# Optimization experiments

Hardware: AMD Instinct MI355X
Metric: run time of the kernel (lower is better)

## Reference

```python
import jax, jax.numpy as jnp
import numpy as np

NODE_NUM = 1_000_000
TYPE_NUM = 4
DIM = 128
L = 80
K = 5
M = 5
B = 256
LK = L - K  # 75


def setup_inputs() -> dict:
    key = jax.random.key(0)
    ks = jax.random.split(key, 8)
    walk = jax.random.randint(ks[0], (B, LK), 0, NODE_NUM)
    pos = jax.random.randint(ks[1], (B, LK, K), 0, NODE_NUM)
    neg = jax.random.randint(ks[2], (B, LK, K, M), 0, NODE_NUM)
    walk_type = jax.random.randint(ks[3], (B, LK), 0, TYPE_NUM)
    pos_type = jax.random.randint(ks[4], (B, LK, K), 0, TYPE_NUM)
    neg_type = jax.random.randint(ks[5], (B, LK, K, M), 0, TYPE_NUM)
    node_embedding = 0.1 * jax.random.normal(ks[6], (NODE_NUM, DIM), dtype=jnp.float32)
    relationship_embedding = jax.random.normal(ks[7], (TYPE_NUM * TYPE_NUM, DIM), dtype=jnp.float32)
    return {
        'walk': walk, 'pos': pos, 'neg': neg,
        'walk_type': walk_type, 'pos_type': pos_type, 'neg_type': neg_type,
        'node_embedding': node_embedding,
        'relationship_embedding': relationship_embedding,
    }


def reference(walk, pos, neg, walk_type, pos_type, neg_type, node_embedding, relationship_embedding):
    T = TYPE_NUM
    # pair type indices into relationship table
    pos_pair_type = T * walk_type[:, :, None] + pos_type               # [B,LK,K]
    neg_pair_type = T * walk_type[:, :, None, None] + neg_type          # [B,LK,K,M]
    pos_pair = relationship_embedding[pos_pair_type]                    # [B,LK,K,D]
    neg_pair = relationship_embedding[neg_pair_type]                    # [B,LK,K,M,D]
    # per-offset pair-type ids (offset by window position k)
    ar = jnp.arange(K)
    pos_pair_type_out = T * T * ar[None, None, :] + pos_pair_type       # [B,LK,K]
    neg_pair_type_out = T * T * ar[None, None, :, None] + neg_pair_type  # [B,LK,K,M]
    # flatten K*M negative dim
    neg_flat = neg.reshape(B, LK, K * M)
    neg_pair = neg_pair.reshape(B, LK, K * M, DIM)
    # embedding gathers
    walk_e = node_embedding[walk]        # [B,LK,D]
    pos_e = node_embedding[pos]          # [B,LK,K,D]
    neg_e = node_embedding[neg_flat]     # [B,LK,K*M,D]
    # sigmoid gate + dot product against walk embedding
    pos_g = pos_e * jax.nn.sigmoid(pos_pair)
    neg_g = neg_e * jax.nn.sigmoid(neg_pair)
    pos_score = jnp.einsum('bld,blkd->blk', walk_e, pos_g).reshape(-1)
    neg_score = jnp.einsum('bld,blkd->blk', walk_e, neg_g).reshape(-1)
    return (pos_score, neg_score, pos_pair_type_out.reshape(-1), neg_pair_type_out.reshape(-1))
```

## Files before the change

### kernel.cpp

```cpp
#include <hip/hip_runtime.h>
#include <math.h>

constexpr int NODE_NUM = 1000000;
constexpr int TYPE_NUM = 4;
constexpr int DIM      = 128;
constexpr int K        = 5;
constexpr int M        = 5;
constexpr int B        = 256;
constexpr int LK       = 75;
constexpr int NBL      = B * LK;
constexpr int PS       = NBL * K;
constexpr int NS       = NBL * K * M;


__global__ __launch_bounds__(256) void skipgram_kernel(
    const int*   __restrict__ walk,
    const int*   __restrict__ pos,
    const int*   __restrict__ neg,
    const int*   __restrict__ walk_type,
    const int*   __restrict__ pos_type,
    const int*   __restrict__ neg_type,
    const float* __restrict__ node_emb,
    const float* __restrict__ rel_emb,
    float*       __restrict__ out)
{
    __shared__ float sig[TYPE_NUM * TYPE_NUM * DIM];
    const int tid = threadIdx.x;
    for (int i = tid; i < TYPE_NUM * TYPE_NUM * DIM; i += 256) {
        const float x = rel_emb[i];
        sig[i] = 1.0f / (1.0f + expf(-x));
    }
    __syncthreads();

    const int wave = tid >> 6;
    const int lane = tid & 63;
    const int half = lane >> 5;
    const int hl   = lane & 31;

    int idx = blockIdx.x * 4 + wave;
    idx = __builtin_amdgcn_readfirstlane(idx);

    const int wnode = walk[idx];
    const int wt    = walk_type[idx];

    const float4 we = *(const float4*)(node_emb + (size_t)wnode * DIM + 4 * hl);


    int tpA[15], tpB[15];
    #pragma unroll
    for (int j = 0; j < 15; ++j) {
        const int r0 = 2 * j, r1 = 2 * j + 1;
        tpA[j] = (r0 < K) ? pos_type[idx * K + r0] : neg_type[idx * K * M + r0 - K];
        tpB[j] = (r1 < K) ? pos_type[idx * K + r1] : neg_type[idx * K * M + r1 - K];
    }

    float4 ev[15];
    #pragma unroll
    for (int j = 0; j < 15; ++j) {
        const int r0 = 2 * j, r1 = 2 * j + 1;
        const int i0 = (r0 < K) ? pos[idx * K + r0] : neg[idx * K * M + r0 - K];
        const int i1 = (r1 < K) ? pos[idx * K + r1] : neg[idx * K * M + r1 - K];
        const int myid = half ? i1 : i0;
        ev[j] = *(const float4*)(node_emb + (size_t)myid * DIM + 4 * hl);
    }

    float p[15];
    #pragma unroll
    for (int j = 0; j < 15; ++j) {
        const int mypt = half ? tpB[j] : tpA[j];
        const float4 sg = *(const float4*)(&sig[(TYPE_NUM * wt + mypt) * DIM + 4 * hl]);
        p[j] = we.x * sg.x * ev[j].x + we.y * sg.y * ev[j].y
             + we.z * sg.z * ev[j].z + we.w * sg.w * ev[j].w;
    }

    #pragma unroll
    for (int j = 0; j < 15; ++j) {
        float v = p[j];
        #pragma unroll
        for (int m2 = 16; m2 >= 1; m2 >>= 1) v += __shfl_xor(v, m2, 64);
        p[j] = v;
    }

    #pragma unroll
    for (int j = 0; j < 15; ++j) {
        const int r    = 2 * j + half;
        const int mytp = half ? tpB[j] : tpA[j];
        if (hl == 0) {
            if (r < K) {
                out[idx * K + r]           = p[j];
                out[PS + NS + idx * K + r] = (float)(TYPE_NUM * TYPE_NUM * r + TYPE_NUM * wt + mytp);
            } else {
                const int rr = r - K;
                const int k  = rr / M;
                out[PS + idx * K * M + rr]           = p[j];
                out[PS + NS + PS + idx * K * M + rr] = (float)(TYPE_NUM * TYPE_NUM * k + TYPE_NUM * wt + mytp);
            }
        }
    }
}

extern "C" void kernel_launch(void* const* d_in, const int* in_sizes, int n_in,
                              void* d_out, int out_size, void* d_ws, size_t ws_size,
                              hipStream_t stream) {
    const int*   walk      = (const int*)d_in[0];
    const int*   pos       = (const int*)d_in[1];
    const int*   neg       = (const int*)d_in[2];
    const int*   walk_type = (const int*)d_in[3];
    const int*   pos_type  = (const int*)d_in[4];
    const int*   neg_type  = (const int*)d_in[5];
    const float* node_emb  = (const float*)d_in[6];
    const float* rel_emb   = (const float*)d_in[7];
    float* out = (float*)d_out;

    const int blocks = NBL / 4;
    skipgram_kernel<<<blocks, 256, 0, stream>>>(
        walk, pos, neg, walk_type, pos_type, neg_type, node_emb, rel_emb, out);
}
```

Before: 54.36 us.

## Software-pipeline embedding gathers in batches and raise occupancy hint

Splits the 15 per-wave gathers into three batches of five, issuing the next batch's loads before computing and reducing the previous one. This lowers live registers, and launch_bounds(256,6) asks the compiler to fit more waves per SIMD so that more memory latency can be hidden. The pair-type offset is folded into the preloaded type array. The risk is that the original code already kept all 15 loads in flight, so the staged issue may shrink memory-level parallelism per wave, and the tighter register cap could cause spills.

```diff
diff --git a/kernel.cpp b/kernel.cpp
--- a/kernel.cpp
+++ b/kernel.cpp
@@ -13,7 +13,52 @@
 constexpr int NS       = NBL * K * M;
 
 
-__global__ __launch_bounds__(256) void skipgram_kernel(
+
+template<int J0>
+__device__ __forceinline__ void issue_batch(
+    const float* __restrict__ node_emb,
+    const int* __restrict__ idxs,
+    int half, int hl, float4 ev[5])
+{
+    #pragma unroll
+    for (int j = 0; j < 5; ++j) {
+        const int r0 = 2 * (J0 + j), r1 = r0 + 1;
+        const int myid = half ? idxs[r1] : idxs[r0];
+        ev[j] = *(const float4*)(node_emb + (size_t)myid * DIM + 4 * hl);
+    }
+}
+
+template<int J0>
+__device__ __forceinline__ void compute_batch(
+    const float* __restrict__ sig,
+    const int* __restrict__ tps,
+    int half, int hl, const float4& we, const float4 ev[5],
+    int idx, float* __restrict__ out)
+{
+    #pragma unroll
+    for (int j = 0; j < 5; ++j) {
+        const int r    = 2 * (J0 + j) + half;
+        const int mytp = half ? tps[2 * (J0 + j) + 1] : tps[2 * (J0 + j)];
+        const float4 sg = *(const float4*)(&sig[mytp * DIM + 4 * hl]);
+        float v = we.x * sg.x * ev[j].x + we.y * sg.y * ev[j].y
+                + we.z * sg.z * ev[j].z + we.w * sg.w * ev[j].w;
+        #pragma unroll
+        for (int m2 = 16; m2 >= 1; m2 >>= 1) v += __shfl_xor(v, m2, 64);
+        if (hl == 0) {
+            if (r < K) {
+                out[idx * K + r]           = v;
+                out[PS + NS + idx * K + r] = (float)(TYPE_NUM * TYPE_NUM * r + mytp);
+            } else {
+                const int rr = r - K;
+                const int k  = rr / M;
+                out[PS + idx * K * M + rr]           = v;
+                out[PS + NS + PS + idx * K * M + rr] = (float)(TYPE_NUM * TYPE_NUM * k + mytp);
+            }
+        }
+    }
+}
+
+__global__ __launch_bounds__(256, 6) void skipgram_kernel(
     const int*   __restrict__ walk,
     const int*   __restrict__ pos,
     const int*   __restrict__ neg,
@@ -43,60 +88,27 @@
     const int wnode = walk[idx];
     const int wt    = walk_type[idx];
 
+    int idxs[30], tps[30];
+    #pragma unroll
+    for (int r = 0; r < 30; ++r) {
+        if (r < K) {
+            idxs[r] = pos[idx * K + r];
+            tps[r]  = TYPE_NUM * wt + pos_type[idx * K + r];
+        } else {
+            idxs[r] = neg[idx * K * M + r - K];
+            tps[r]  = TYPE_NUM * wt + neg_type[idx * K * M + r - K];
+        }
+    }
+
     const float4 we = *(const float4*)(node_emb + (size_t)wnode * DIM + 4 * hl);
 
-
-    int tpA[15], tpB[15];
-    #pragma unroll
-    for (int j = 0; j < 15; ++j) {
-        const int r0 = 2 * j, r1 = 2 * j + 1;
-        tpA[j] = (r0 < K) ? pos_type[idx * K + r0] : neg_type[idx * K * M + r0 - K];
-        tpB[j] = (r1 < K) ? pos_type[idx * K + r1] : neg_type[idx * K * M + r1 - K];
-    }
-
-    float4 ev[15];
-    #pragma unroll
-    for (int j = 0; j < 15; ++j) {
-        const int r0 = 2 * j, r1 = 2 * j + 1;
-        const int i0 = (r0 < K) ? pos[idx * K + r0] : neg[idx * K * M + r0 - K];
-        const int i1 = (r1 < K) ? pos[idx * K + r1] : neg[idx * K * M + r1 - K];
-        const int myid = half ? i1 : i0;
-        ev[j] = *(const float4*)(node_emb + (size_t)myid * DIM + 4 * hl);
-    }
-
-    float p[15];
-    #pragma unroll
-    for (int j = 0; j < 15; ++j) {
-        const int mypt = half ? tpB[j] : tpA[j];
-        const float4 sg = *(const float4*)(&sig[(TYPE_NUM * wt + mypt) * DIM + 4 * hl]);
-        p[j] = we.x * sg.x * ev[j].x + we.y * sg.y * ev[j].y
-             + we.z * sg.z * ev[j].z + we.w * sg.w * ev[j].w;
-    }
-
-    #pragma unroll
-    for (int j = 0; j < 15; ++j) {
-        float v = p[j];
-        #pragma unroll
-        for (int m2 = 16; m2 >= 1; m2 >>= 1) v += __shfl_xor(v, m2, 64);
-        p[j] = v;
-    }
-
-    #pragma unroll
-    for (int j = 0; j < 15; ++j) {
-        const int r    = 2 * j + half;
-        const int mytp = half ? tpB[j] : tpA[j];
-        if (hl == 0) {
-            if (r < K) {
-                out[idx * K + r]           = p[j];
-                out[PS + NS + idx * K + r] = (float)(TYPE_NUM * TYPE_NUM * r + TYPE_NUM * wt + mytp);
-            } else {
-                const int rr = r - K;
-                const int k  = rr / M;
-                out[PS + idx * K * M + rr]           = p[j];
-                out[PS + NS + PS + idx * K * M + rr] = (float)(TYPE_NUM * TYPE_NUM * k + TYPE_NUM * wt + mytp);
-            }
-        }
-    }
+    float4 evA[5], evB[5], evC[5];
+    issue_batch<0>(node_emb, idxs, half, hl, evA);
+    issue_batch<5>(node_emb, idxs, half, hl, evB);
+    compute_batch<0>(sig, tps, half, hl, we, evA, idx, out);
+    issue_batch<10>(node_emb, idxs, half, hl, evC);
+    compute_batch<5>(sig, tps, half, hl, we, evB, idx, out);
+    compute_batch<10>(sig, tps, half, hl, we, evC, idx, out);
 }
 
 extern "C" void kernel_launch(void* const* d_in, const int* in_sizes, int n_in,
```

Result: slower. 56.63 us (+4.2%).

## Replace shared-memory sigmoid table with per-wave register gate selection

Applied to the files above, without the earlier changes.

Drops the per-block shared-memory sigmoid table over all 2048 relationship entries and the __syncthreads that guarded it. Each wave now loads only the four relationship rows for its walk type, applies sigmoid with fast __expf, and pre-multiplies them with the walk embedding. The right gated vector for each context node is then picked with register selects instead of LDS reads. This removes the 2048-element setup and block barrier from every block. In exchange it uses more registers and per-element selects, and __expf gives slightly different rounding than expf.

```diff
diff --git a/kernel.cpp b/kernel.cpp
--- a/kernel.cpp
+++ b/kernel.cpp
@@ -13,6 +13,7 @@
 constexpr int NS       = NBL * K * M;
 
 
+
 __global__ __launch_bounds__(256) void skipgram_kernel(
     const int*   __restrict__ walk,
     const int*   __restrict__ pos,
@@ -24,14 +25,7 @@
     const float* __restrict__ rel_emb,
     float*       __restrict__ out)
 {
-    __shared__ float sig[TYPE_NUM * TYPE_NUM * DIM];
-    const int tid = threadIdx.x;
-    for (int i = tid; i < TYPE_NUM * TYPE_NUM * DIM; i += 256) {
-        const float x = rel_emb[i];
-        sig[i] = 1.0f / (1.0f + expf(-x));
-    }
-    __syncthreads();
-
+    const int tid  = threadIdx.x;
     const int wave = tid >> 6;
     const int lane = tid & 63;
     const int half = lane >> 5;
@@ -43,57 +37,70 @@
     const int wnode = walk[idx];
     const int wt    = walk_type[idx];
 
-    const float4 we = *(const float4*)(node_emb + (size_t)wnode * DIM + 4 * hl);
-
-
-    int tpA[15], tpB[15];
+    int idxs[30], st[30];
     #pragma unroll
-    for (int j = 0; j < 15; ++j) {
-        const int r0 = 2 * j, r1 = 2 * j + 1;
-        tpA[j] = (r0 < K) ? pos_type[idx * K + r0] : neg_type[idx * K * M + r0 - K];
-        tpB[j] = (r1 < K) ? pos_type[idx * K + r1] : neg_type[idx * K * M + r1 - K];
+    for (int r = 0; r < 30; ++r) {
+        if (r < K) {
+            idxs[r] = pos[idx * K + r];
+            st[r]   = pos_type[idx * K + r];
+        } else {
+            idxs[r] = neg[idx * K * M + r - K];
+            st[r]   = neg_type[idx * K * M + r - K];
+        }
     }
 
+    const float4 we = *(const float4*)(node_emb + (size_t)wnode * DIM + 4 * hl);
     float4 ev[15];
     #pragma unroll
     for (int j = 0; j < 15; ++j) {
-        const int r0 = 2 * j, r1 = 2 * j + 1;
-        const int i0 = (r0 < K) ? pos[idx * K + r0] : neg[idx * K * M + r0 - K];
-        const int i1 = (r1 < K) ? pos[idx * K + r1] : neg[idx * K * M + r1 - K];
-        const int myid = half ? i1 : i0;
+        const int myid = half ? idxs[2 * j + 1] : idxs[2 * j];
         ev[j] = *(const float4*)(node_emb + (size_t)myid * DIM + 4 * hl);
     }
 
-    float p[15];
+    float4 sgt[4];
     #pragma unroll
-    for (int j = 0; j < 15; ++j) {
-        const int mypt = half ? tpB[j] : tpA[j];
-        const float4 sg = *(const float4*)(&sig[(TYPE_NUM * wt + mypt) * DIM + 4 * hl]);
-        p[j] = we.x * sg.x * ev[j].x + we.y * sg.y * ev[j].y
-             + we.z * sg.z * ev[j].z + we.w * sg.w * ev[j].w;
+    for (int t = 0; t < 4; ++t) {
+        const float4 x = *(const float4*)(rel_emb + (size_t)(TYPE_NUM * wt + t) * DIM + 4 * hl);
+        sgt[t].x = 1.0f / (1.0f + __expf(-x.x));
+        sgt[t].y = 1.0f / (1.0f + __expf(-x.y));
+        sgt[t].z = 1.0f / (1.0f + __expf(-x.z));
+        sgt[t].w = 1.0f / (1.0f + __expf(-x.w));
+    }
+
+    float4 wg[4];
+    #pragma unroll
+    for (int t = 0; t < 4; ++t) {
+        wg[t].x = we.x * sgt[t].x; wg[t].y = we.y * sgt[t].y;
+        wg[t].z = we.z * sgt[t].z; wg[t].w = we.w * sgt[t].w;
     }
 
     #pragma unroll
     for (int j = 0; j < 15; ++j) {
-        float v = p[j];
+        const int myst = half ? st[2 * j + 1] : st[2 * j];
+        const bool lo = (myst & 1), hi = (myst & 2);
+        float4 a, b, g;
+        a.x = lo ? wg[1].x : wg[0].x; a.y = lo ? wg[1].y : wg[0].y;
+        a.z = lo ? wg[1].z : wg[0].z; a.w = lo ? wg[1].w : wg[0].w;
+        b.x = lo ? wg[3].x : wg[2].x; b.y = lo ? wg[3].y : wg[2].y;
+        b.z = lo ? wg[3].z : wg[2].z; b.w = lo ? wg[3].w : wg[2].w;
+        g.x = hi ? b.x : a.x; g.y = hi ? b.y : a.y;
+        g.z = hi ? b.z : a.z; g.w = hi ? b.w : a.w;
+
+        float v = g.x * ev[j].x + g.y * ev[j].y + g.z * ev[j].z + g.w * ev[j].w;
         #pragma unroll
         for (int m2 = 16; m2 >= 1; m2 >>= 1) v += __shfl_xor(v, m2, 64);
-        p[j] = v;
-    }
 
-    #pragma unroll
-    for (int j = 0; j < 15; ++j) {
         const int r    = 2 * j + half;
-        const int mytp = half ? tpB[j] : tpA[j];
+        const int mytp = TYPE_NUM * wt + myst;
         if (hl == 0) {
             if (r < K) {
-                out[idx * K + r]           = p[j];
-                out[PS + NS + idx * K + r] = (float)(TYPE_NUM * TYPE_NUM * r + TYPE_NUM * wt + mytp);
+                out[idx * K + r]           = v;
+                out[PS + NS + idx * K + r] = (float)(TYPE_NUM * TYPE_NUM * r + mytp);
             } else {
                 const int rr = r - K;
                 const int k  = rr / M;
-                out[PS + idx * K * M + rr]           = p[j];
-                out[PS + NS + PS + idx * K * M + rr] = (float)(TYPE_NUM * TYPE_NUM * k + TYPE_NUM * wt + mytp);
+                out[PS + idx * K * M + rr]           = v;
+                out[PS + NS + PS + idx * K * M + rr] = (float)(TYPE_NUM * TYPE_NUM * k + mytp);
             }
         }
     }
```

Result: slower. 144.9 us (+166.5%).
